# Kernel tuning notes

Hardware: AMD Instinct MI355X
Metric: run time of the kernel (lower is better)

## Reference

```python
import jax, jax.numpy as jnp
import numpy as np

D = 1024

def setup_inputs() -> dict:
    key = jax.random.key(0)
    kx, kw = jax.random.split(key)
    x = jax.random.normal(kx, (4, 2048, D), dtype=jnp.float32)
    # nn.Linear(d, 3d, bias=False): weight [3d, d]; y = x @ W.T
    W = jax.random.normal(kw, (3 * D, D), dtype=jnp.float32) * (1.0 / np.sqrt(D))
    return {"x": x, "W": W}

def reference(x, W):
    d = x.shape[-1]
    qkv = jnp.einsum('bsd,ed->bse', x, W)  # [B,S,3d]
    q, k, v = jnp.split(qkv, 3, axis=2)
    att = jnp.einsum('bqd,bkd->bqk', q, k) * (1.0 / jnp.sqrt(jnp.asarray(d, x.dtype)))
    att = jax.nn.softmax(att, axis=-1)
    y = jnp.einsum('bqk,bkd->bqd', att, v)
    return y
```

## Files before the change

kernel.cpp:

```cpp
#include <hip/hip_runtime.h>
#include <hip/hip_bf16.h>

typedef __attribute__((ext_vector_type(8))) short short8;
typedef __attribute__((ext_vector_type(4))) float f32x4;

typedef unsigned short u16;

__device__ __forceinline__ u16 f32_to_bf16(float f) {
    unsigned int u = __float_as_uint(f);
    u += 0x7fffu + ((u >> 16) & 1u);
    return (u16)(u >> 16);
}

__device__ __forceinline__ void gload16(const u16* g, u16* lds_base) {
    __builtin_amdgcn_global_load_lds(
        (const __attribute__((address_space(1))) void*)g,
        (__attribute__((address_space(3))) void*)lds_base, 16, 0, 0);
}

__device__ __forceinline__ void phase_bar() {
    __builtin_amdgcn_s_barrier();
    __builtin_amdgcn_sched_barrier(0);
}
__device__ __forceinline__ void wait_vm8() {
    asm volatile("s_waitcnt vmcnt(8)" ::: "memory");
    __builtin_amdgcn_sched_barrier(0);
}
__device__ __forceinline__ void wait_vm7() {
    asm volatile("s_waitcnt vmcnt(7)" ::: "memory");
    __builtin_amdgcn_sched_barrier(0);
}
__device__ __forceinline__ void wait_vm0() {
    asm volatile("s_waitcnt vmcnt(0)" ::: "memory");
    __builtin_amdgcn_sched_barrier(0);
}

__global__ void cast_inputs(const float* __restrict__ x, u16* __restrict__ Xb,
                            const float* __restrict__ W, u16* __restrict__ Wb,
                            float* __restrict__ l,
                            int nx4, int nw4, int nl) {
    int i = blockIdx.x * blockDim.x + threadIdx.x;
    if (i >= nx4 + nw4) {
        int idx = i - (nx4 + nw4);
        if (idx < nl) l[idx] = 0.f;
        return;
    }
    const float* in; u16* out; int idx;
    if (i < nx4) { in = x; out = Xb; idx = i; }
    else { idx = i - nx4; in = W; out = Wb; }
    float4 v = ((const float4*)in)[idx];
    ushort4 o;
    o.x = f32_to_bf16(v.x); o.y = f32_to_bf16(v.y);
    o.z = f32_to_bf16(v.z); o.w = f32_to_bf16(v.w);
    ((ushort4*)out)[idx] = o;
}


struct Acc256 { f32x4 acc[8][4]; };
struct Acc192 { f32x4 acc[8][3]; };

template<int MH>
__device__ __forceinline__ void rd_a(const u16* __restrict__ sA, int wr, int lane,
                                     int lr, short8 (&af)[4][2]) {
#pragma unroll
    for (int a2 = 0; a2 < 4; ++a2) {
        const int row = wr * 128 + MH * 64 + a2 * 16 + lr;
#pragma unroll
        for (int k2 = 0; k2 < 2; ++k2) {
            const int cb = (lane >> 4) + k2 * 4;
            af[a2][k2] = *(const short8*)(sA + row * 64 + ((cb ^ (lr & 7)) * 8));
        }
    }
}

template<int NH>
__device__ __forceinline__ void rd_b(const u16* __restrict__ sB, int wc, int lane,
                                     int lr, short8 (&bf)[2][2]) {
#pragma unroll
    for (int b2 = 0; b2 < 2; ++b2) {
        const int row = wc * 64 + NH * 32 + b2 * 16 + lr;
#pragma unroll
        for (int k2 = 0; k2 < 2; ++k2) {
            const int cb = (lane >> 4) + k2 * 4;
            bf[b2][k2] = *(const short8*)(sB + row * 64 + ((cb ^ (lr & 7)) * 8));
        }
    }
}

template<int MH, int NH>
__device__ __forceinline__ void mm_q(Acc256& fr, const short8 (&af)[4][2],
                                     const short8 (&bf)[2][2]) {
    __builtin_amdgcn_s_setprio(1);
#pragma unroll
    for (int a2 = 0; a2 < 4; ++a2)
#pragma unroll
        for (int b2 = 0; b2 < 2; ++b2)
#pragma unroll
            for (int k2 = 0; k2 < 2; ++k2)
                fr.acc[MH * 4 + a2][NH * 2 + b2] =
                    __builtin_amdgcn_mfma_f32_16x16x32_bf16(
                        af[a2][k2], bf[b2][k2],
                        fr.acc[MH * 4 + a2][NH * 2 + b2], 0, 0, 0);
    __builtin_amdgcn_s_setprio(0);
}

__device__ __forceinline__ void rd_b01(const u16* __restrict__ sB, int wc, int lane,
                                       int lr, short8 (&bf)[2][2]) {
#pragma unroll
    for (int b2 = 0; b2 < 2; ++b2) {
        const int row = wc * 48 + b2 * 16 + lr;
#pragma unroll
        for (int k2 = 0; k2 < 2; ++k2) {
            const int cb = (lane >> 4) + k2 * 4;
            bf[b2][k2] = *(const short8*)(sB + row * 64 + ((cb ^ (lr & 7)) * 8));
        }
    }
}

__device__ __forceinline__ void rd_b2(const u16* __restrict__ sB, int wc, int lane,
                                      int lr, short8 (&bf)[2]) {
    const int row = wc * 48 + 32 + lr;
#pragma unroll
    for (int k2 = 0; k2 < 2; ++k2) {
        const int cb = (lane >> 4) + k2 * 4;
        bf[k2] = *(const short8*)(sB + row * 64 + ((cb ^ (lr & 7)) * 8));
    }
}

template<int MH>
__device__ __forceinline__ void mm_b01(Acc192& fr, const short8 (&af)[4][2],
                                       const short8 (&bf)[2][2]) {
    __builtin_amdgcn_s_setprio(1);
#pragma unroll
    for (int a2 = 0; a2 < 4; ++a2)
#pragma unroll
        for (int b2 = 0; b2 < 2; ++b2)
#pragma unroll
            for (int k2 = 0; k2 < 2; ++k2)
                fr.acc[MH * 4 + a2][b2] =
                    __builtin_amdgcn_mfma_f32_16x16x32_bf16(
                        af[a2][k2], bf[b2][k2],
                        fr.acc[MH * 4 + a2][b2], 0, 0, 0);
    __builtin_amdgcn_s_setprio(0);
}

template<int MH>
__device__ __forceinline__ void mm_b2(Acc192& fr, const short8 (&af)[4][2],
                                      const short8 (&bf)[2]) {
    __builtin_amdgcn_s_setprio(1);
#pragma unroll
    for (int a2 = 0; a2 < 4; ++a2)
#pragma unroll
        for (int k2 = 0; k2 < 2; ++k2)
            fr.acc[MH * 4 + a2][2] =
                __builtin_amdgcn_mfma_f32_16x16x32_bf16(
                    af[a2][k2], bf[k2], fr.acc[MH * 4 + a2][2], 0, 0, 0);
    __builtin_amdgcn_s_setprio(0);
}

__device__ __forceinline__ void gemm_core_256(
    const u16* __restrict__ A, const u16* __restrict__ Bt,
    int K, int lda, int ldb, int row0, int col0, u16* sm, Acc256& fr)
{
    const int t    = threadIdx.x;
    const int lane = t & 63;
    const int wave = t >> 6;
    const int wr   = wave >> 2;
    const int wc   = wave & 3;
    const int lr   = lane & 15;
    const int srow = lane >> 3;
    const int gc   = (lane & 7) ^ srow;

    const u16* const sA0 = sm;
    const u16* const sA1 = sm + 16384;
    const u16* const sB0 = sm + 32768;
    const u16* const sB1 = sm + 49152;

#pragma unroll
    for (int a = 0; a < 8; ++a)
#pragma unroll
        for (int b = 0; b < 4; ++b)
            fr.acc[a][b] = (f32x4){0.f, 0.f, 0.f, 0.f};

    const u16* aB = A  + (long long)(row0 + wave * 8 + srow) * lda + gc * 8;
    const u16* bB = Bt + (long long)(col0 + wave * 8 + srow) * ldb + gc * 8;
    u16* const sAw = sm + wave * 512;
    u16* const sBw = sm + 32768 + wave * 512;

    auto stageA = [&](int kt) {
        u16* d = sAw + (kt & 1) * 16384;
        const u16* g = aB + kt * 64;
#pragma unroll
        for (int r4 = 0; r4 < 4; ++r4)
            gload16(g + (long long)(r4 * 64) * lda, d + r4 * 4096);
    };
    auto stageB = [&](int kt) {
        u16* d = sBw + (kt & 1) * 16384;
        const u16* g = bB + kt * 64;
#pragma unroll
        for (int r4 = 0; r4 < 4; ++r4)
            gload16(g + (long long)(r4 * 64) * ldb, d + r4 * 4096);
    };

    stageA(0); stageB(0); stageA(1); stageB(1);
    wait_vm8();
    phase_bar();

    const int NI = K >> 7;
    short8 af[4][2], bfa[2][2], bfb[2][2];
#pragma unroll 1
    for (int i = 0; i < NI; ++i) {
        const bool more = (i + 1 < NI);
        const int t2 = 2 * i + 2;

        rd_a<0>(sA0, wr, lane, lr, af);
        rd_b<0>(sB0, wc, lane, lr, bfa);
        phase_bar();
        mm_q<0, 0>(fr, af, bfa);
        phase_bar();

        rd_b<1>(sB0, wc, lane, lr, bfb);
        phase_bar();
        mm_q<0, 1>(fr, af, bfb);
        phase_bar();

        rd_a<1>(sA0, wr, lane, lr, af);
        if (more) stageB(t2);
        phase_bar();
        mm_q<1, 1>(fr, af, bfb);
        phase_bar();

        if (more) stageA(t2);
        phase_bar();
        mm_q<1, 0>(fr, af, bfa);
        if (more) wait_vm8(); else wait_vm0();
        phase_bar();

        rd_a<0>(sA1, wr, lane, lr, af);
        rd_b<0>(sB1, wc, lane, lr, bfa);
        phase_bar();
        mm_q<0, 0>(fr, af, bfa);
        phase_bar();

        rd_b<1>(sB1, wc, lane, lr, bfb);
        phase_bar();
        mm_q<0, 1>(fr, af, bfb);
        phase_bar();

        rd_a<1>(sA1, wr, lane, lr, af);
        if (more) stageB(t2 + 1);
        phase_bar();
        mm_q<1, 1>(fr, af, bfb);
        phase_bar();

        if (more) stageA(t2 + 1);
        phase_bar();
        mm_q<1, 0>(fr, af, bfa);
        if (more) wait_vm8();
        phase_bar();
    }
}

__device__ __forceinline__ void gemm_core_192(
    const u16* __restrict__ A, const u16* __restrict__ Bt,
    int K, int lda, int ldb, int row0, int col0, u16* sm, Acc192& fr)
{
    const int t    = threadIdx.x;
    const int lane = t & 63;
    const int wave = t >> 6;
    const int wr   = wave >> 2;
    const int wc   = wave & 3;
    const int lr   = lane & 15;
    const int srow = lane >> 3;
    const int gc   = (lane & 7) ^ srow;

    const u16* const sA0 = sm;
    const u16* const sA1 = sm + 16384;
    const u16* const sB0 = sm + 32768;
    const u16* const sB1 = sm + 45056;

#pragma unroll
    for (int a = 0; a < 8; ++a)
#pragma unroll
        for (int b = 0; b < 3; ++b)
            fr.acc[a][b] = (f32x4){0.f, 0.f, 0.f, 0.f};

    const u16* aB = A  + (long long)(row0 + wave * 8 + srow) * lda + gc * 8;
    const u16* bB = Bt + (long long)(col0 + wave * 8 + srow) * ldb + gc * 8;
    u16* const sAw = sm + wave * 512;
    u16* const sBw = sm + 32768 + wave * 512;

    auto stageA = [&](int kt) {
        u16* d = sAw + (kt & 1) * 16384;
        const u16* g = aB + kt * 64;
#pragma unroll
        for (int r4 = 0; r4 < 4; ++r4)
            gload16(g + (long long)(r4 * 64) * lda, d + r4 * 4096);
    };
    auto stageB = [&](int kt) {
        u16* d = sBw + (kt & 1) * 12288;
        const u16* g = bB + kt * 64;
#pragma unroll
        for (int r4 = 0; r4 < 3; ++r4)
            gload16(g + (long long)(r4 * 64) * ldb, d + r4 * 4096);
    };

    stageA(0); stageB(0); stageA(1); stageB(1);
    wait_vm7();
    phase_bar();

    const int NI = K >> 7;
    short8 af[4][2], bfa[2][2], bfb[2];
#pragma unroll 1
    for (int i = 0; i < NI; ++i) {
        const bool more = (i + 1 < NI);
        const int t2 = 2 * i + 2;

        rd_a<0>(sA0, wr, lane, lr, af);
        rd_b01(sB0, wc, lane, lr, bfa);
        phase_bar();
        mm_b01<0>(fr, af, bfa);
        phase_bar();

        rd_b2(sB0, wc, lane, lr, bfb);
        phase_bar();
        mm_b2<0>(fr, af, bfb);
        phase_bar();

        rd_a<1>(sA0, wr, lane, lr, af);
        if (more) stageB(t2);
        phase_bar();
        mm_b2<1>(fr, af, bfb);
        phase_bar();

        if (more) stageA(t2);
        phase_bar();
        mm_b01<1>(fr, af, bfa);
        if (more) wait_vm7(); else wait_vm0();
        phase_bar();

        rd_a<0>(sA1, wr, lane, lr, af);
        rd_b01(sB1, wc, lane, lr, bfa);
        phase_bar();
        mm_b01<0>(fr, af, bfa);
        phase_bar();

        rd_b2(sB1, wc, lane, lr, bfb);
        phase_bar();
        mm_b2<0>(fr, af, bfb);
        phase_bar();

        rd_a<1>(sA1, wr, lane, lr, af);
        if (more) stageB(t2 + 1);
        phase_bar();
        mm_b2<1>(fr, af, bfb);
        phase_bar();

        if (more) stageA(t2 + 1);
        phase_bar();
        mm_b01<1>(fr, af, bfa);
        if (more) wait_vm7();
        phase_bar();
    }
}


__global__ __launch_bounds__(512, 1) void gemm_qkv(
    const u16* __restrict__ Xb, const u16* __restrict__ Wb,
    u16* __restrict__ QK, u16* __restrict__ VT)
{
    __shared__ u16 sm[57344];
    const int row0 = blockIdx.y * 256;
    const int col0 = blockIdx.x * 192;

    Acc192 fr;
    gemm_core_192(Xb, Wb, 1024, 1024, 1024, row0, col0, sm, fr);

    const int lane = threadIdx.x & 63;
    const int wave = threadIdx.x >> 6;
    const int wr = wave >> 2, wc = wave & 3;
    const int cr = (lane >> 4) * 4, cc = lane & 15;

#pragma unroll
    for (int a = 0; a < 8; ++a) {
        const int grow = row0 + wr * 128 + a * 16 + cr;
#pragma unroll
        for (int b = 0; b < 3; ++b) {
            const int gcol = col0 + wc * 48 + b * 16 + cc;
            if (gcol < 2048) {
#pragma unroll
                for (int r = 0; r < 4; ++r)
                    QK[(long long)(grow + r) * 2048 + gcol] =
                        f32_to_bf16(fr.acc[a][b][r]);
            } else {
                const int bz = grow >> 11, s = grow & 2047;
                const int d = gcol - 2048;
                ushort4 o;
                o.x = f32_to_bf16(fr.acc[a][b][0]);
                o.y = f32_to_bf16(fr.acc[a][b][1]);
                o.z = f32_to_bf16(fr.acc[a][b][2]);
                o.w = f32_to_bf16(fr.acc[a][b][3]);
                *(ushort4*)(&VT[((long long)(bz * 1024 + d)) * 2048 + s]) = o;
            }
        }
    }
}

__global__ __launch_bounds__(512, 1) void gemm_s_exp(
    const u16* __restrict__ QK, u16* __restrict__ E, float* __restrict__ l)
{
    __shared__ u16 sm[65536];
    const long long boff = (long long)blockIdx.z * 2048 * 2048;
    const u16* Q  = QK + boff;
    const u16* Kp = QK + boff + 1024;
    u16* Eb = E + boff;
    float* lb = l + (long long)blockIdx.z * 2048;
    const int row0 = blockIdx.y * 256;
    const int col0 = blockIdx.x * 256;

    Acc256 fr;
    gemm_core_256(Q, Kp, 1024, 2048, 2048, row0, col0, sm, fr);

    const int lane = threadIdx.x & 63;
    const int wave = threadIdx.x >> 6;
    const int wr = wave >> 2, wc = wave & 3;
    const int cr = (lane >> 4) * 4, cc = lane & 15;

#pragma unroll
    for (int a = 0; a < 8; ++a) {
        float rs[4] = {0.f, 0.f, 0.f, 0.f};
#pragma unroll
        for (int b = 0; b < 4; ++b)
#pragma unroll
            for (int r = 0; r < 4; ++r) {
                float e = __expf(fr.acc[a][b][r] * 0.03125f);
                rs[r] += e;
                int grow = row0 + wr * 128 + a * 16 + cr + r;
                int gcol = col0 + wc * 64 + b * 16 + cc;
                Eb[(long long)grow * 2048 + gcol] = f32_to_bf16(e);
            }
#pragma unroll
        for (int r = 0; r < 4; ++r) {
#pragma unroll
            for (int m = 1; m < 16; m <<= 1) rs[r] += __shfl_xor(rs[r], m, 64);
            if ((lane & 15) == 0)
                atomicAdd(&lb[row0 + wr * 128 + a * 16 + cr + r], rs[r]);
        }
    }
}

__global__ __launch_bounds__(512, 1) void gemm_pv_sk(
    const u16* __restrict__ E, const u16* __restrict__ VT,
    float* __restrict__ P0, float* __restrict__ P1)
{
    __shared__ u16 sm[65536];
    const int qt = blockIdx.x;
    const int dt = blockIdx.y & 3;
    const int ks = blockIdx.y >> 2;
    const u16* Eb  = E  + (long long)blockIdx.z * 2048 * 2048 + ks * 1024;
    const u16* VTb = VT + (long long)blockIdx.z * 1024 * 2048 + ks * 1024;
    float* Pb = (ks ? P1 : P0) + (long long)blockIdx.z * 2048 * 1024;

    Acc256 fr;
    gemm_core_256(Eb, VTb, 1024, 2048, 2048, qt * 256, dt * 256, sm, fr);

    const int lane = threadIdx.x & 63;
    const int wave = threadIdx.x >> 6;
    const int wr = wave >> 2, wc = wave & 3;
    const int cr = (lane >> 4) * 4, cc = lane & 15;
#pragma unroll
    for (int a = 0; a < 8; ++a) {
        const int q = qt * 256 + wr * 128 + a * 16 + cr;
#pragma unroll
        for (int b = 0; b < 4; ++b) {
            const int d = dt * 256 + wc * 64 + b * 16 + cc;
#pragma unroll
            for (int r = 0; r < 4; ++r)
                Pb[(long long)(q + r) * 1024 + d] = fr.acc[a][b][r];
        }
    }
}

__global__ void reduce_pv(float* __restrict__ out, const float* __restrict__ part,
                          const float* __restrict__ l) {
    const int i = blockIdx.x * blockDim.x + threadIdx.x;
    const int e0 = i << 2;
    const int q  = (e0 >> 10) & 2047;
    const int z  = e0 >> 21;
    const float linv = 1.0f / l[z * 2048 + q];
    float4 a = ((const float4*)out)[i];
    float4 b = ((const float4*)part)[i];
    float4 o = {(a.x + b.x) * linv, (a.y + b.y) * linv,
                (a.z + b.z) * linv, (a.w + b.w) * linv};
    ((float4*)out)[i] = o;
}

extern "C" void kernel_launch(void* const* d_in, const int* in_sizes, int n_in,
                              void* d_out, int out_size, void* d_ws, size_t ws_size,
                              hipStream_t stream) {
    const float* x = (const float*)d_in[0];
    const float* W = (const float*)d_in[1];
    float* out = (float*)d_out;

    char* ws = (char*)d_ws;
    u16*   Xb = (u16*)(ws);
    u16*   Wb = (u16*)(ws + 16777216LL);
    u16*   QK = (u16*)(ws + 23068672LL);
    u16*   VT = (u16*)(ws + 56623104LL);
    u16*   E  = (u16*)(ws + 73400320LL);
    float* l  = (float*)(ws + 106954752LL);

    const int nx4 = 8192 * 1024 / 4, nw4 = 3072 * 1024 / 4;
    cast_inputs<<<11296, 256, 0, stream>>>(x, Xb, W, Wb, l, nx4, nw4, 8192);
    gemm_qkv<<<dim3(16, 32, 1), 512, 0, stream>>>(Xb, Wb, QK, VT);
    gemm_s_exp<<<dim3(8, 8, 4), 512, 0, stream>>>(QK, E, l);
    gemm_pv_sk<<<dim3(8, 8, 4), 512, 0, stream>>>(E, VT, out, (float*)QK);
    reduce_pv<<<8192, 256, 0, stream>>>(out, (float*)QK, l);
}
```

Before: 244.1 us.

## Replace split-K PV GEMM plus reduce with full-K 256x128 tile GEMM and fused normalization

Drops the split-K PV GEMM, which wrote two partial fp32 outputs that a separate reduce kernel then summed and normalized. It is replaced by one full-K GEMM using a 256x128 output tile with its own pipelined core, and the 1/l row normalization is applied in the epilogue. This removes the partial-sum write and read traffic and one kernel launch, while keeping the same 256-block grid. The barrier helpers are also reworked so that sched_barrier sits only before the closing barrier, and it is removed from the vmcnt waits, giving the compiler more freedom to schedule. The trade-off is a K loop twice as long per block and a lower MFMA-to-load ratio from the narrower N tile.

```diff
diff --git a/kernel.cpp b/kernel.cpp
--- a/kernel.cpp
+++ b/kernel.cpp
@@ -18,21 +18,22 @@
         (__attribute__((address_space(3))) void*)lds_base, 16, 0, 0);
 }
 
-__device__ __forceinline__ void phase_bar() {
+__device__ __forceinline__ void bar() { __builtin_amdgcn_s_barrier(); }
+__device__ __forceinline__ void bar_end() {
+    __builtin_amdgcn_sched_barrier(0);
     __builtin_amdgcn_s_barrier();
-    __builtin_amdgcn_sched_barrier(0);
 }
 __device__ __forceinline__ void wait_vm8() {
     asm volatile("s_waitcnt vmcnt(8)" ::: "memory");
-    __builtin_amdgcn_sched_barrier(0);
 }
 __device__ __forceinline__ void wait_vm7() {
     asm volatile("s_waitcnt vmcnt(7)" ::: "memory");
-    __builtin_amdgcn_sched_barrier(0);
+}
+__device__ __forceinline__ void wait_vm6() {
+    asm volatile("s_waitcnt vmcnt(6)" ::: "memory");
 }
 __device__ __forceinline__ void wait_vm0() {
     asm volatile("s_waitcnt vmcnt(0)" ::: "memory");
-    __builtin_amdgcn_sched_barrier(0);
 }
 
 __global__ void cast_inputs(const float* __restrict__ x, u16* __restrict__ Xb,
@@ -58,6 +59,7 @@
 
 struct Acc256 { f32x4 acc[8][4]; };
 struct Acc192 { f32x4 acc[8][3]; };
+struct Acc128 { f32x4 acc[8][2]; };
 
 template<int MH>
 __device__ __forceinline__ void rd_a(const u16* __restrict__ sA, int wr, int lane,
@@ -155,6 +157,36 @@
             fr.acc[MH * 4 + a2][2] =
                 __builtin_amdgcn_mfma_f32_16x16x32_bf16(
                     af[a2][k2], bf[k2], fr.acc[MH * 4 + a2][2], 0, 0, 0);
+    __builtin_amdgcn_s_setprio(0);
+}
+
+__device__ __forceinline__ void rd_bb(const u16* __restrict__ sB, int wc, int lane,
+                                      int lr, short8 (&bf)[2][2]) {
+#pragma unroll
+    for (int b2 = 0; b2 < 2; ++b2) {
+        const int row = wc * 32 + b2 * 16 + lr;
+#pragma unroll
+        for (int k2 = 0; k2 < 2; ++k2) {
+            const int cb = (lane >> 4) + k2 * 4;
+            bf[b2][k2] = *(const short8*)(sB + row * 64 + ((cb ^ (lr & 7)) * 8));
+        }
+    }
+}
+
+template<int MH>
+__device__ __forceinline__ void mm_n128(Acc128& fr, const short8 (&af)[4][2],
+                                        const short8 (&bf)[2][2]) {
+    __builtin_amdgcn_s_setprio(1);
+#pragma unroll
+    for (int a2 = 0; a2 < 4; ++a2)
+#pragma unroll
+        for (int b2 = 0; b2 < 2; ++b2)
+#pragma unroll
+            for (int k2 = 0; k2 < 2; ++k2)
+                fr.acc[MH * 4 + a2][b2] =
+                    __builtin_amdgcn_mfma_f32_16x16x32_bf16(
+                        af[a2][k2], bf[b2][k2],
+                        fr.acc[MH * 4 + a2][b2], 0, 0, 0);
     __builtin_amdgcn_s_setprio(0);
 }
 
@@ -204,7 +236,7 @@
 
     stageA(0); stageB(0); stageA(1); stageB(1);
     wait_vm8();
-    phase_bar();
+    bar();
 
     const int NI = K >> 7;
     short8 af[4][2], bfa[2][2], bfb[2][2];
@@ -215,49 +247,49 @@
 
         rd_a<0>(sA0, wr, lane, lr, af);
         rd_b<0>(sB0, wc, lane, lr, bfa);
-        phase_bar();
+        bar();
         mm_q<0, 0>(fr, af, bfa);
-        phase_bar();
+        bar_end();
 
         rd_b<1>(sB0, wc, lane, lr, bfb);
-        phase_bar();
+        bar();
         mm_q<0, 1>(fr, af, bfb);
-        phase_bar();
+        bar_end();
 
         rd_a<1>(sA0, wr, lane, lr, af);
         if (more) stageB(t2);
-        phase_bar();
+        bar();
         mm_q<1, 1>(fr, af, bfb);
-        phase_bar();
+        bar_end();
 
         if (more) stageA(t2);
-        phase_bar();
+        bar();
         mm_q<1, 0>(fr, af, bfa);
         if (more) wait_vm8(); else wait_vm0();
-        phase_bar();
+        bar_end();
 
         rd_a<0>(sA1, wr, lane, lr, af);
         rd_b<0>(sB1, wc, lane, lr, bfa);
-        phase_bar();
+        bar();
         mm_q<0, 0>(fr, af, bfa);
-        phase_bar();
+        bar_end();
 
         rd_b<1>(sB1, wc, lane, lr, bfb);
-        phase_bar();
+        bar();
         mm_q<0, 1>(fr, af, bfb);
-        phase_bar();
+        bar_end();
 
         rd_a<1>(sA1, wr, lane, lr, af);
         if (more) stageB(t2 + 1);
-        phase_bar();
+        bar();
         mm_q<1, 1>(fr, af, bfb);
-        phase_bar();
+        bar_end();
 
         if (more) stageA(t2 + 1);
-        phase_bar();
+        bar();
         mm_q<1, 0>(fr, af, bfa);
         if (more) wait_vm8();
-        phase_bar();
+        bar_end();
     }
 }
 
@@ -307,7 +339,7 @@
 
     stageA(0); stageB(0); stageA(1); stageB(1);
     wait_vm7();
-    phase_bar();
+    bar();
 
     const int NI = K >> 7;
     short8 af[4][2], bfa[2][2], bfb[2];
@@ -318,49 +350,134 @@
 
         rd_a<0>(sA0, wr, lane, lr, af);
         rd_b01(sB0, wc, lane, lr, bfa);
-        phase_bar();
+        bar();
         mm_b01<0>(fr, af, bfa);
-        phase_bar();
+        bar_end();
 
         rd_b2(sB0, wc, lane, lr, bfb);
-        phase_bar();
+        bar();
         mm_b2<0>(fr, af, bfb);
-        phase_bar();
+        bar_end();
 
         rd_a<1>(sA0, wr, lane, lr, af);
         if (more) stageB(t2);
-        phase_bar();
+        bar();
         mm_b2<1>(fr, af, bfb);
-        phase_bar();
+        bar_end();
 
         if (more) stageA(t2);
-        phase_bar();
+        bar();
         mm_b01<1>(fr, af, bfa);
         if (more) wait_vm7(); else wait_vm0();
-        phase_bar();
+        bar_end();
 
         rd_a<0>(sA1, wr, lane, lr, af);
         rd_b01(sB1, wc, lane, lr, bfa);
-        phase_bar();
+        bar();
         mm_b01<0>(fr, af, bfa);
-        phase_bar();
+        bar_end();
 
         rd_b2(sB1, wc, lane, lr, bfb);
-        phase_bar();
+        bar();
         mm_b2<0>(fr, af, bfb);
-        phase_bar();
+        bar_end();
 
         rd_a<1>(sA1, wr, lane, lr, af);
         if (more) stageB(t2 + 1);
-        phase_bar();
+        bar();
         mm_b2<1>(fr, af, bfb);
-        phase_bar();
+        bar_end();
 
         if (more) stageA(t2 + 1);
-        phase_bar();
+        bar();
         mm_b01<1>(fr, af, bfa);
         if (more) wait_vm7();
-        phase_bar();
+        bar_end();
+    }
+}
+
+__device__ __forceinline__ void gemm_core_n128(
+    const u16* __restrict__ A, const u16* __restrict__ Bt,
+    int K, int lda, int ldb, int row0, int col0, u16* sm, Acc128& fr)
+{
+    const int t    = threadIdx.x;
+    const int lane = t & 63;
+    const int wave = t >> 6;
+    const int wr   = wave >> 2;
+    const int wc   = wave & 3;
+    const int lr   = lane & 15;
+    const int srow = lane >> 3;
+    const int gc   = (lane & 7) ^ srow;
+
+    const u16* const sA0 = sm;
+    const u16* const sA1 = sm + 16384;
+    const u16* const sB0 = sm + 32768;
+    const u16* const sB1 = sm + 40960;
+
+#pragma unroll
+    for (int a = 0; a < 8; ++a)
+#pragma unroll
+        for (int b = 0; b < 2; ++b)
+            fr.acc[a][b] = (f32x4){0.f, 0.f, 0.f, 0.f};
+
+    const u16* aB = A  + (long long)(row0 + wave * 8 + srow) * lda + gc * 8;
+    const u16* bB = Bt + (long long)(col0 + wave * 8 + srow) * ldb + gc * 8;
+    u16* const sAw = sm + wave * 512;
+    u16* const sBw = sm + 32768 + wave * 512;
+
+    auto stageA = [&](int kt) {
+        u16* d = sAw + (kt & 1) * 16384;
+        const u16* g = aB + kt * 64;
+#pragma unroll
+        for (int r4 = 0; r4 < 4; ++r4)
+            gload16(g + (long long)(r4 * 64) * lda, d + r4 * 4096);
+    };
+    auto stageB = [&](int kt) {
+        u16* d = sBw + (kt & 1) * 8192;
+        const u16* g = bB + kt * 64;
+#pragma unroll
+        for (int r4 = 0; r4 < 2; ++r4)
+            gload16(g + (long long)(r4 * 64) * ldb, d + r4 * 4096);
+    };
+
+    stageB(0); stageA(0); stageB(1); stageA(1);
+    wait_vm6();
+    bar();
+
+    const int NI = K >> 7;
+    short8 af[4][2], bf[2][2];
+#pragma unroll 1
+    for (int i = 0; i < NI; ++i) {
+        const bool more = (i + 1 < NI);
+        const int t2 = 2 * i + 2;
+
+        rd_a<0>(sA0, wr, lane, lr, af);
+        rd_bb(sB0, wc, lane, lr, bf);
+        if (more) stageB(t2);
+        bar();
+        mm_n128<0>(fr, af, bf);
+        bar_end();
+
+        rd_a<1>(sA0, wr, lane, lr, af);
+        if (more) stageA(t2);
+        bar();
+        mm_n128<1>(fr, af, bf);
+        if (more) wait_vm6(); else wait_vm0();
+        bar_end();
+
+        rd_a<0>(sA1, wr, lane, lr, af);
+        rd_bb(sB1, wc, lane, lr, bf);
+        if (more) stageB(t2 + 1);
+        bar();
+        mm_n128<0>(fr, af, bf);
+        bar_end();
+
+        rd_a<1>(sA1, wr, lane, lr, af);
+        if (more) stageA(t2 + 1);
+        bar();
+        mm_n128<1>(fr, af, bf);
+        if (more) wait_vm6();
+        bar_end();
     }
 }
 
@@ -449,50 +566,41 @@
     }
 }
 
-__global__ __launch_bounds__(512, 1) void gemm_pv_sk(
+__global__ __launch_bounds__(512, 1) void gemm_pv(
     const u16* __restrict__ E, const u16* __restrict__ VT,
-    float* __restrict__ P0, float* __restrict__ P1)
+    const float* __restrict__ l, float* __restrict__ Y)
 {
-    __shared__ u16 sm[65536];
-    const int qt = blockIdx.x;
-    const int dt = blockIdx.y & 3;
-    const int ks = blockIdx.y >> 2;
-    const u16* Eb  = E  + (long long)blockIdx.z * 2048 * 2048 + ks * 1024;
-    const u16* VTb = VT + (long long)blockIdx.z * 1024 * 2048 + ks * 1024;
-    float* Pb = (ks ? P1 : P0) + (long long)blockIdx.z * 2048 * 1024;
-
-    Acc256 fr;
-    gemm_core_256(Eb, VTb, 1024, 2048, 2048, qt * 256, dt * 256, sm, fr);
+    __shared__ u16 sm[49152];
+    const u16* Eb  = E  + (long long)blockIdx.z * 2048 * 2048;
+    const u16* VTb = VT + (long long)blockIdx.z * 1024 * 2048;
+    const float* lb = l + (long long)blockIdx.z * 2048;
+    float* Yb = Y + (long long)blockIdx.z * 2048 * 1024;
+    const int row0 = blockIdx.x * 256;
+    const int col0 = blockIdx.y * 128;
+
+    Acc128 fr;
+    gemm_core_n128(Eb, VTb, 2048, 2048, 2048, row0, col0, sm, fr);
 
     const int lane = threadIdx.x & 63;
     const int wave = threadIdx.x >> 6;
     const int wr = wave >> 2, wc = wave & 3;
     const int cr = (lane >> 4) * 4, cc = lane & 15;
+
 #pragma unroll
     for (int a = 0; a < 8; ++a) {
-        const int q = qt * 256 + wr * 128 + a * 16 + cr;
-#pragma unroll
-        for (int b = 0; b < 4; ++b) {
-            const int d = dt * 256 + wc * 64 + b * 16 + cc;
-#pragma unroll
-            for (int r = 0; r < 4; ++r)
-                Pb[(long long)(q + r) * 1024 + d] = fr.acc[a][b][r];
+        const int q0 = row0 + wr * 128 + a * 16 + cr;
+        const float4 l4 = *(const float4*)(&lb[q0]);
+        const float inv0 = 1.0f / l4.x, inv1 = 1.0f / l4.y;
+        const float inv2 = 1.0f / l4.z, inv3 = 1.0f / l4.w;
+#pragma unroll
+        for (int b = 0; b < 2; ++b) {
+            const int d = col0 + wc * 32 + b * 16 + cc;
+            Yb[(long long)(q0 + 0) * 1024 + d] = fr.acc[a][b][0] * inv0;
+            Yb[(long long)(q0 + 1) * 1024 + d] = fr.acc[a][b][1] * inv1;
+            Yb[(long long)(q0 + 2) * 1024 + d] = fr.acc[a][b][2] * inv2;
+            Yb[(long long)(q0 + 3) * 1024 + d] = fr.acc[a][b][3] * inv3;
         }
     }
-}
-
-__global__ void reduce_pv(float* __restrict__ out, const float* __restrict__ part,
-                          const float* __restrict__ l) {
-    const int i = blockIdx.x * blockDim.x + threadIdx.x;
-    const int e0 = i << 2;
-    const int q  = (e0 >> 10) & 2047;
-    const int z  = e0 >> 21;
-    const float linv = 1.0f / l[z * 2048 + q];
-    float4 a = ((const float4*)out)[i];
-    float4 b = ((const float4*)part)[i];
-    float4 o = {(a.x + b.x) * linv, (a.y + b.y) * linv,
-                (a.z + b.z) * linv, (a.w + b.w) * linv};
-    ((float4*)out)[i] = o;
 }
 
 extern "C" void kernel_launch(void* const* d_in, const int* in_sizes, int n_in,
@@ -514,6 +622,5 @@
     cast_inputs<<<11296, 256, 0, stream>>>(x, Xb, W, Wb, l, nx4, nw4, 8192);
     gemm_qkv<<<dim3(16, 32, 1), 512, 0, stream>>>(Xb, Wb, QK, VT);
     gemm_s_exp<<<dim3(8, 8, 4), 512, 0, stream>>>(QK, E, l);
-    gemm_pv_sk<<<dim3(8, 8, 4), 512, 0, stream>>>(E, VT, out, (float*)QK);
-    reduce_pv<<<8192, 256, 0, stream>>>(out, (float*)QK, l);
-}
+    gemm_pv<<<dim3(8, 8, 4), 512, 0, stream>>>(E, VT, l, out);
+}
```

Result: faster. 222.9 us (-8.7%).
